# Kernel optimization log

Measured on AMD Instinct MI355X. Metric: run time of the kernel, lower is better.

Reference implementation:

```python
import jax, jax.numpy as jnp
import numpy as np

H = 19  # input_size == hidden_size

def setup_inputs() -> dict:
    key = jax.random.key(0)
    ks = jax.random.split(key, 7)
    seq_len, batch = 2048, 1024
    s = 1.0 / np.sqrt(H)  # PyTorch default uniform(-1/sqrt(H), 1/sqrt(H))
    x = jax.random.normal(ks[0], (seq_len, batch, H), dtype=jnp.float32)
    W_ih = jax.random.uniform(ks[1], (3 * H, H), jnp.float32, -s, s)
    W_hh = jax.random.uniform(ks[2], (3 * H, H), jnp.float32, -s, s)
    b_ih = jax.random.uniform(ks[3], (3 * H,), jnp.float32, -s, s)
    b_hh = jax.random.uniform(ks[4], (3 * H,), jnp.float32, -s, s)
    W_out = jax.random.uniform(ks[5], (1, H), jnp.float32, -s, s)
    b_out = jax.random.uniform(ks[6], (1,), jnp.float32, -s, s)
    return {"x": x, "W_ih": W_ih, "W_hh": W_hh, "b_ih": b_ih,
            "b_hh": b_hh, "W_out": W_out, "b_out": b_out}

def _gru(x, W_ih, W_hh, b_ih, b_hh):
    # Precompute all input projections in one big GEMM: [T, B, 3H]
    xg = jnp.einsum('tbi,gi->tbg', x, W_ih) + b_ih
    Whr, Whz, Whn = W_hh[:H], W_hh[H:2*H], W_hh[2*H:]
    bhr, bhz, bhn = b_hh[:H], b_hh[H:2*H], b_hh[2*H:]
    h0 = jnp.zeros(x.shape[1:2] + (H,), dtype=x.dtype)

    def step(h, xg_t):
        xr, xz, xn = xg_t[:, :H], xg_t[:, H:2*H], xg_t[:, 2*H:]
        r = jax.nn.sigmoid(xr + h @ Whr.T + bhr)
        z = jax.nn.sigmoid(xz + h @ Whz.T + bhz)
        n = jnp.tanh(xn + r * (h @ Whn.T + bhn))
        h_new = (1.0 - z) * n + z * h
        return h_new, h_new

    _, r_out = jax.lax.scan(step, h0, xg)  # r_out: [T, B, H]
    return r_out

def reference(x, W_ih, W_hh, b_ih, b_hh, W_out, b_out):
    r_out = _gru(x, W_ih, W_hh, b_ih, b_hh)
    return r_out @ W_out.T + b_out  # [T, B, 1]
```

## Files before the change

kernel.cpp:

```cpp
#include <hip/hip_runtime.h>
#include <math.h>

#define HH 19
#define NG 57
#define SL 64
#define NB 1024
#define TT 2048

typedef float v2f __attribute__((ext_vector_type(2)));
typedef float v4f __attribute__((ext_vector_type(4)));
typedef unsigned u2 __attribute__((ext_vector_type(2)));

__device__ __forceinline__ float rlf(float v, int l) {
  return __uint_as_float(__builtin_amdgcn_readlane(__float_as_uint(v), l));
}
__device__ __forceinline__ float frcp(float v) { return __builtin_amdgcn_rcpf(v); }
__device__ __forceinline__ float fexp2(float v) {
#if __has_builtin(__builtin_amdgcn_exp2f)
  return __builtin_amdgcn_exp2f(v);
#else
  return exp2f(v);
#endif
}
__device__ __forceinline__ unsigned short f2h(float f) {
  return __builtin_bit_cast(unsigned short, (_Float16)f);
}
__device__ __forceinline__ float h2f(unsigned short u) {
  return (float)__builtin_bit_cast(_Float16, u);
}
__device__ __forceinline__ v2f mk2(float a, float b) { v2f r; r.x = a; r.y = b; return r; }
__device__ __forceinline__ v2f vfma(v2f a, v2f b, v2f c) {
#if __has_builtin(__builtin_elementwise_fma)
  return __builtin_elementwise_fma(a, b, c);
#else
  v2f r; r.x = fmaf(a.x, b.x, c.x); r.y = fmaf(a.y, b.y, c.y); return r;
#endif
}

#if __has_builtin(__builtin_amdgcn_permlane32_swap)
#define HAVE_PLS 1
__device__ __forceinline__ u2 pls(float x) {
  unsigned u = __float_as_uint(x);
  return __builtin_amdgcn_permlane32_swap(u, u, false, false);
}
#else
#define HAVE_PLS 0
#endif

__global__ __launch_bounds__(256) void xg_proj3(
    const float* __restrict__ x, const float* __restrict__ Wih,
    const float* __restrict__ bih, const float* __restrict__ bhh,
    unsigned short* __restrict__ xg)
{
  const int lane = threadIdx.x & 63;
  const int wv = __builtin_amdgcn_readfirstlane((int)(threadIdx.x >> 6));
  const int g = lane < NG ? lane : NG - 1;
  const float L2E = 1.4426950408889634f;
  const float scale = (g < 2 * HH) ? -L2E : 2.0f * L2E;

  float w[HH];
#pragma unroll
  for (int k = 0; k < HH; ++k) w[k] = Wih[g * HH + k] * scale;
  const float cbv = (bih[g] + (g < 2 * HH ? bhh[g] : 0.0f)) * scale;

  const size_t pair0 = ((size_t)blockIdx.x * 4 + wv) * 64;
  for (int p = 0; p < 64; ++p) {
    const size_t pair = pair0 + p;
    const float* __restrict__ xr = x + pair * HH;
    float a = cbv;
#pragma unroll
    for (int k = 0; k < HH; ++k) a = fmaf(xr[k], w[k], a);
    xg[pair * SL + lane] = f2h(a);
  }
}

__global__ void __launch_bounds__(64)
__attribute__((amdgpu_waves_per_eu(1, 1)))
gru_rec3(const unsigned short* __restrict__ xg, const float* __restrict__ Whh,
         const float* __restrict__ bhh, const float* __restrict__ Wout,
         const float* __restrict__ bout, float* __restrict__ out)
{
  __shared__ __align__(16) float hsh[64];
  const int b = blockIdx.x;
  const int lane = threadIdx.x;
  const float L2E = 1.4426950408889634f;

  int row;
  if (lane < 32)      row = lane;
  else if (lane < 51) row = lane + 6;
  else if (lane < 57) row = lane - 19;
  else                row = 37;
  const bool isn = (row >= 2 * HH);
  const float s = isn ? (2.0f * L2E) : -L2E;

  v2f wh2[10], wo2[10];
#pragma unroll
  for (int j = 0; j < 10; ++j) {
    const int k0 = 2 * j, k1 = 2 * j + 1;
    wh2[j].x = s * Whh[row * HH + k0];
    wh2[j].y = (k1 < HH) ? s * Whh[row * HH + k1] : 0.0f;
    wo2[j].x = Wout[k0];
    wo2[j].y = (k1 < HH) ? Wout[k1] : 0.0f;
  }
  const float dinit = isn ? (2.0f * L2E * bhh[row]) : 0.0f;
  const float bo = bout[0];

  const int il = lane < HH ? lane : HH - 1;
  const int zaddr = ((il < 13) ? (19 + il) : (38 + il)) * 4;

#if HAVE_PLS
  bool loIsX;
  {
    unsigned l = (unsigned)lane;
    u2 pr = __builtin_amdgcn_permlane32_swap(l, l, false, false);
    loIsX = ((unsigned)__builtin_amdgcn_readlane((int)pr.x, 32) < 32u);
  }
#define LOBCAST(val, dst) do { u2 _s = pls(val);                        \
    dst = __uint_as_float(loIsX ? _s.x : _s.y); } while (0)
#define HIBCAST(val, dst) do { u2 _s = pls(val);                        \
    dst = __uint_as_float(loIsX ? _s.y : _s.x); } while (0)
#else
  const int loaddr = (lane & 31) * 4;
  const int hiaddr = ((lane & 31) | 32) * 4;
#define LOBCAST(val, dst) dst = __uint_as_float((unsigned)              \
    __builtin_amdgcn_ds_bpermute(loaddr, (int)__float_as_uint(val)))
#define HIBCAST(val, dst) dst = __uint_as_float((unsigned)              \
    __builtin_amdgcn_ds_bpermute(hiaddr, (int)__float_as_uint(val)))
#endif

  float h = 0.0f;
  v2f shA[10], shB[10];
#pragma unroll
  for (int j = 0; j < 10; ++j) { shA[j] = mk2(0.f, 0.f); shB[j] = mk2(0.f, 0.f); }

  const unsigned short* __restrict__ xb = xg + (size_t)b * SL + row;
#define LOADX(dst, trow) do { dst = xb[(size_t)(trow) * (NB * SL)]; } while (0)

  unsigned short s0, s1, s2, s3, s4, s5, s6, s7;
  LOADX(s0, 0); LOADX(s1, 1); LOADX(s2, 2); LOADX(s3, 3);
  LOADX(s4, 4); LOADX(s5, 5); LOADX(s6, 6); LOADX(s7, 7);

#define OPROJ(sh, ovar) do {                                            \
    v2f _oA = mk2(bo, 0.f), _oB = mk2(0.f, 0.f);                        \
    _Pragma("unroll")                                                   \
    for (int _j = 0; _j < 5; ++_j)  _oA = vfma(sh[_j], wo2[_j], _oA);   \
    _Pragma("unroll")                                                   \
    for (int _j = 5; _j < 10; ++_j) _oB = vfma(sh[_j], wo2[_j], _oB);   \
    const v2f _ov = _oA + _oB;                                          \
    ovar = _ov.x + _ov.y;                                               \
  } while (0)

#define BODY(tcur, slot, shC, shP, ovar) do {                           \
     \
    hsh[lane] = (lane < HH) ? h : 0.0f;                                 \
    const v4f q0 = *(const v4f*)&hsh[0];                                \
    const v4f q1 = *(const v4f*)&hsh[4];                                \
    const v4f q2 = *(const v4f*)&hsh[8];                                \
    const v4f q3 = *(const v4f*)&hsh[12];                               \
    const v4f q4 = *(const v4f*)&hsh[16];                               \
    const float xv = h2f(slot);                                         \
    { const int _tl = ((tcur) + 8 < TT) ? (tcur) + 8 : TT - 1;          \
      LOADX(slot, _tl); }                                               \
                     \
    OPROJ(shP, ovar);                                                   \
    shC[0] = mk2(q0.x, q0.y); shC[1] = mk2(q0.z, q0.w);                 \
    shC[2] = mk2(q1.x, q1.y); shC[3] = mk2(q1.z, q1.w);                 \
    shC[4] = mk2(q2.x, q2.y); shC[5] = mk2(q2.z, q2.w);                 \
    shC[6] = mk2(q3.x, q3.y); shC[7] = mk2(q3.z, q3.w);                 \
    shC[8] = mk2(q4.x, q4.y); shC[9] = mk2(q4.z, q4.w);                 \
                                \
    v2f _a0 = mk2(dinit, 0.f), _a1 = mk2(0.f, 0.f);                     \
    _Pragma("unroll")                                                   \
    for (int _j = 0; _j < 5; ++_j)  _a0 = vfma(shC[_j], wh2[_j], _a0);  \
    _Pragma("unroll")                                                   \
    for (int _j = 5; _j < 10; ++_j) _a1 = vfma(shC[_j], wh2[_j], _a1);  \
    const v2f _av = _a0 + _a1;                                          \
    const float preh = _av.x + _av.y;                                   \
    const float pre  = xv + preh;                        \
    const float sig  = frcp(fexp2(pre) + 1.0f);                         \
    const int zzi = __builtin_amdgcn_ds_bpermute(                       \
        zaddr, (int)__float_as_uint(sig));                              \
    float rr; LOBCAST(sig, rr);                                         \
    const float arg = fmaf(rr, preh, xv);                  \
    const float nn = fmaf(-2.0f, frcp(fexp2(arg) + 1.0f), 1.0f);        \
    float nh; HIBCAST(nn, nh);                                          \
    const float zz = __uint_as_float((unsigned)zzi);                    \
    h = fmaf(zz, h - nh, nh);                                           \
  } while (0)

  float o0, o1, o2, o3, o4, o5, o6, o7;
  float* __restrict__ ob = out + b;

  for (int t = 0; t < TT; t += 8) {
    BODY(t + 0, s0, shA, shB, o0);
    BODY(t + 1, s1, shB, shA, o1);
    BODY(t + 2, s2, shA, shB, o2);
    BODY(t + 3, s3, shB, shA, o3);
    BODY(t + 4, s4, shA, shB, o4);
    BODY(t + 5, s5, shB, shA, o5);
    BODY(t + 6, s6, shA, shB, o6);
    BODY(t + 7, s7, shB, shA, o7);
    if (lane == 0) {
      ob[(size_t)(t >= 2 ? t - 2 : 0) * NB] = o0;
      ob[(size_t)(t >= 1 ? t - 1 : 0) * NB] = o1;
      ob[(size_t)(t + 0) * NB] = o2;
      ob[(size_t)(t + 1) * NB] = o3;
      ob[(size_t)(t + 2) * NB] = o4;
      ob[(size_t)(t + 3) * NB] = o5;
      ob[(size_t)(t + 4) * NB] = o6;
      ob[(size_t)(t + 5) * NB] = o7;
    }
  }

  float oe;
  OPROJ(shB, oe);
  if (lane == 0) ob[(size_t)(TT - 2) * NB] = oe;
  hsh[lane] = (lane < HH) ? h : 0.0f;
  {
    const v4f q0 = *(const v4f*)&hsh[0];
    const v4f q1 = *(const v4f*)&hsh[4];
    const v4f q2 = *(const v4f*)&hsh[8];
    const v4f q3 = *(const v4f*)&hsh[12];
    const v4f q4 = *(const v4f*)&hsh[16];
    shA[0] = mk2(q0.x, q0.y); shA[1] = mk2(q0.z, q0.w);
    shA[2] = mk2(q1.x, q1.y); shA[3] = mk2(q1.z, q1.w);
    shA[4] = mk2(q2.x, q2.y); shA[5] = mk2(q2.z, q2.w);
    shA[6] = mk2(q3.x, q3.y); shA[7] = mk2(q3.z, q3.w);
    shA[8] = mk2(q4.x, q4.y); shA[9] = mk2(q4.z, q4.w);
    OPROJ(shA, oe);
    if (lane == 0) ob[(size_t)(TT - 1) * NB] = oe;
  }
#undef LOADX
#undef BODY
#undef OPROJ
#undef LOBCAST
#undef HIBCAST
}

__global__ void __launch_bounds__(64)
__attribute__((amdgpu_waves_per_eu(1, 1)))
gru57_v4(const float* __restrict__ x, const float* __restrict__ Wih,
         const float* __restrict__ Whh, const float* __restrict__ bih,
         const float* __restrict__ bhh, const float* __restrict__ Wout,
         const float* __restrict__ bout, float* __restrict__ out)
{
  const int b = blockIdx.x;
  const int lane = threadIdx.x;
  const float L2E = 1.4426950408889634f;

  int row;
  if (lane < 32)      row = lane;
  else if (lane < 51) row = lane + 6;
  else if (lane < 57) row = lane - 19;
  else                row = 37;
  const bool isn = (row >= 2 * HH);
  const float scale = isn ? (2.0f * L2E) : L2E;

  v2f wx2[10], wh2[10], wo2[10];
#pragma unroll
  for (int j = 0; j < 10; ++j) {
    const int k0 = 2 * j, k1 = 2 * j + 1;
    wx2[j].x = Wih[row * HH + k0] * scale;
    wx2[j].y = (k1 < HH) ? Wih[row * HH + k1] * scale : 0.0f;
    wh2[j].x = Whh[row * HH + k0] * scale;
    wh2[j].y = (k1 < HH) ? Whh[row * HH + k1] * scale : 0.0f;
    wo2[j].x = Wout[k0];
    wo2[j].y = (k1 < HH) ? Wout[k1] : 0.0f;
  }
  const float bxv = bih[row] * scale, bhv = bhh[row] * scale;
  const float ax0 = isn ? bxv : (bxv + bhv);
  const float ah0 = isn ? bhv : 0.0f;
  const float bo  = bout[0];

  const int il = lane < HH ? lane : HH - 1;
  const int zaddr = ((il < 13) ? (19 + il) : (38 + il)) * 4;

#if HAVE_PLS
  bool loIsX;
  {
    unsigned l = (unsigned)lane;
    u2 pr = __builtin_amdgcn_permlane32_swap(l, l, false, false);
    loIsX = ((unsigned)__builtin_amdgcn_readlane((int)pr.x, 32) < 32u);
  }
#define LOBCAST(val, dst) do { u2 _s = pls(val);                        \
    dst = __uint_as_float(loIsX ? _s.x : _s.y); } while (0)
#define HIBCAST(val, dst) do { u2 _s = pls(val);                        \
    dst = __uint_as_float(loIsX ? _s.y : _s.x); } while (0)
#else
  const int loaddr = (lane & 31) * 4;
  const int hiaddr = ((lane & 31) | 32) * 4;
#define LOBCAST(val, dst) dst = __uint_as_float((unsigned)              \
    __builtin_amdgcn_ds_bpermute(loaddr, (int)__float_as_uint(val)))
#define HIBCAST(val, dst) dst = __uint_as_float((unsigned)              \
    __builtin_amdgcn_ds_bpermute(hiaddr, (int)__float_as_uint(val)))
#endif

  float h = 0.0f;
  v2f sh2[10];
#pragma unroll
  for (int j = 0; j < 10; ++j) sh2[j] = mk2(0.f, 0.f);

  const int kx = lane < HH ? lane : HH - 1;
  const float* __restrict__ xbase = x + (size_t)b * HH + kx;

#define LOADXF(dst, trow) do { dst = xbase[(size_t)(trow) * (NB * HH)]; } while (0)
#define XBCAST(slot, xu) do {                                           \
    _Pragma("unroll")                                                   \
    for (int _j = 0; _j < 9; ++_j) {                                    \
      xu[_j].x = rlf(slot, 2 * _j);                                     \
      xu[_j].y = rlf(slot, 2 * _j + 1);                                 \
    }                                                                   \
    xu[9].x = rlf(slot, 18); xu[9].y = 0.0f;                            \
  } while (0)
#define XDOT(xu, dstvar) do {                                           \
    v2f _aA = mk2(ax0, 0.0f), _aB = mk2(0.0f, 0.0f);                    \
    _Pragma("unroll")                                                   \
    for (int _j = 0; _j < 5; ++_j)  _aA = vfma(xu[_j], wx2[_j], _aA);   \
    _Pragma("unroll")                                                   \
    for (int _j = 5; _j < 10; ++_j) _aB = vfma(xu[_j], wx2[_j], _aB);   \
    const v2f _s = _aA + _aB;                                           \
    dstvar = _s.x + _s.y;                                               \
  } while (0)

  float xlA, xlB, xlC, xlD;
  LOADXF(xlA, 0); LOADXF(xlB, 1); LOADXF(xlC, 2); LOADXF(xlD, 3);
  float prex;
  { v2f xu0[10]; XBCAST(xlA, xu0); XDOT(xu0, prex); }

#define BODYF(tcur, nslot, lslot) do {                                  \
    v2f ahA = mk2(ah0, 0.0f), ahB = mk2(0.0f, 0.0f);                    \
    _Pragma("unroll")                                                   \
    for (int _j = 0; _j < 5; ++_j)  ahA = vfma(sh2[_j], wh2[_j], ahA);  \
    _Pragma("unroll")                                                   \
    for (int _j = 5; _j < 10; ++_j) ahB = vfma(sh2[_j], wh2[_j], ahB);  \
    float prexN;                                                        \
    { v2f _xu[10]; XBCAST(nslot, _xu); XDOT(_xu, prexN); }              \
    { const int _tl = ((tcur) + 4 < TT) ? (tcur) + 4 : TT - 1;          \
      LOADXF(lslot, _tl); }                                             \
    const v2f ahv = ahA + ahB;                                          \
    const float preh = ahv.x + ahv.y;                                   \
    const float pre  = prex + preh;                                     \
    const float sig  = frcp(1.0f + fexp2(-pre));                        \
    const int zzi = __builtin_amdgcn_ds_bpermute(                       \
        zaddr, (int)__float_as_uint(sig));                              \
    float rr; LOBCAST(sig, rr);                                         \
    const float npre = fmaf(rr, preh, prex);                            \
    const float nn = fmaf(-2.0f, frcp(fexp2(npre) + 1.0f), 1.0f);       \
    float nh; HIBCAST(nn, nh);                                          \
    const float zz = __uint_as_float((unsigned)zzi);                    \
    h = fmaf(zz, h - nh, nh);                                           \
    _Pragma("unroll")                                                   \
    for (int _j = 0; _j < 9; ++_j) {                                    \
      sh2[_j].x = rlf(h, 2 * _j);                                       \
      sh2[_j].y = rlf(h, 2 * _j + 1);                                   \
    }                                                                   \
    sh2[9].x = rlf(h, 18); sh2[9].y = 0.0f;                             \
    v2f oA = mk2(bo, 0.0f), oB = mk2(0.0f, 0.0f);                       \
    _Pragma("unroll")                                                   \
    for (int _j = 0; _j < 5; ++_j)  oA = vfma(sh2[_j], wo2[_j], oA);    \
    _Pragma("unroll")                                                   \
    for (int _j = 5; _j < 10; ++_j) oB = vfma(sh2[_j], wo2[_j], oB);    \
    const v2f ov = oA + oB;                                             \
    if (lane == 0) out[(size_t)(tcur) * NB + b] = ov.x + ov.y;          \
    prex = prexN;                                                       \
  } while (0)

  for (int t = 0; t < TT; t += 4) {
    BODYF(t + 0, xlB, xlA);
    BODYF(t + 1, xlC, xlB);
    BODYF(t + 2, xlD, xlC);
    BODYF(t + 3, xlA, xlD);
  }

#undef LOADXF
#undef XBCAST
#undef XDOT
#undef BODYF
#undef LOBCAST
#undef HIBCAST
}

extern "C" void kernel_launch(void* const* d_in, const int* in_sizes, int n_in,
                              void* d_out, int out_size, void* d_ws, size_t ws_size,
                              hipStream_t stream) {
  const float* x    = (const float*)d_in[0];
  const float* Wih  = (const float*)d_in[1];
  const float* Whh  = (const float*)d_in[2];
  const float* bih  = (const float*)d_in[3];
  const float* bhh  = (const float*)d_in[4];
  const float* Wout = (const float*)d_in[5];
  const float* bout = (const float*)d_in[6];
  float* out = (float*)d_out;

  const size_t need = (size_t)TT * NB * SL * sizeof(unsigned short);
  if (ws_size >= need) {
    unsigned short* xgws = (unsigned short*)d_ws;
    xg_proj3<<<dim3((TT * NB) / 256), dim3(256), 0, stream>>>(
        x, Wih, bih, bhh, xgws);
    gru_rec3<<<dim3(NB), dim3(64), 0, stream>>>(
        xgws, Whh, bhh, Wout, bout, out);
  } else {
    gru57_v4<<<dim3(NB), dim3(64), 0, stream>>>(
        x, Wih, Whh, bih, bhh, Wout, bout, out);
  }
}
```

Measured before the change: 627.2 us.

## Restructure GRU recurrence lanes, broadcast h via readlane, stage projection through LDS

The projection kernel now stages x through shared memory, computes all 57 gates per thread (one pair per thread), and writes the result out coalesced through an LDS transpose, instead of reading x row-wise per lane. The recurrence kernel changes its lane mapping: each lane computes both an r/n row and a z row, so z no longer needs a cross-lane bpermute. h is broadcast to all lanes with readlane instead of an LDS store and reload. The output projection runs on the current h, which shifts the store indices by one. The cost is about twice the FMAs per lane and 19 scalar readlanes per step on the serial critical path.

```diff
diff --git a/kernel.cpp b/kernel.cpp
--- a/kernel.cpp
+++ b/kernel.cpp
@@ -8,7 +8,6 @@
 #define TT 2048
 
 typedef float v2f __attribute__((ext_vector_type(2)));
-typedef float v4f __attribute__((ext_vector_type(4)));
 typedef unsigned u2 __attribute__((ext_vector_type(2)));
 
 __device__ __forceinline__ float rlf(float v, int l) {
@@ -47,66 +46,81 @@
 #define HAVE_PLS 0
 #endif
 
-__global__ __launch_bounds__(256) void xg_proj3(
+__global__ __launch_bounds__(256) void xg_proj4(
     const float* __restrict__ x, const float* __restrict__ Wih,
     const float* __restrict__ bih, const float* __restrict__ bhh,
     unsigned short* __restrict__ xg)
 {
-  const int lane = threadIdx.x & 63;
-  const int wv = __builtin_amdgcn_readfirstlane((int)(threadIdx.x >> 6));
-  const int g = lane < NG ? lane : NG - 1;
+  __shared__ __align__(16) float ls[256 * 33];
+  const int tid = threadIdx.x;
+  const size_t pair0 = (size_t)blockIdx.x * 256;
   const float L2E = 1.4426950408889634f;
-  const float scale = (g < 2 * HH) ? -L2E : 2.0f * L2E;
-
-  float w[HH];
-#pragma unroll
-  for (int k = 0; k < HH; ++k) w[k] = Wih[g * HH + k] * scale;
-  const float cbv = (bih[g] + (g < 2 * HH ? bhh[g] : 0.0f)) * scale;
-
-  const size_t pair0 = ((size_t)blockIdx.x * 4 + wv) * 64;
-  for (int p = 0; p < 64; ++p) {
-    const size_t pair = pair0 + p;
-    const float* __restrict__ xr = x + pair * HH;
-    float a = cbv;
-#pragma unroll
-    for (int k = 0; k < HH; ++k) a = fmaf(xr[k], w[k], a);
-    xg[pair * SL + lane] = f2h(a);
+
+  {
+    const float* __restrict__ src = x + pair0 * HH;
+#pragma unroll
+    for (int j = 0; j < HH; ++j) ls[j * 256 + tid] = src[j * 256 + tid];
+  }
+  __syncthreads();
+
+  float xv[HH];
+#pragma unroll
+  for (int k = 0; k < HH; ++k) xv[k] = ls[tid * HH + k];
+  __syncthreads();
+
+  unsigned short* __restrict__ lsh = (unsigned short*)ls;
+#pragma unroll 1
+  for (int g = 0; g < NG; ++g) {
+    float a = bih[g] + ((g < 2 * HH) ? bhh[g] : 0.0f);
+#pragma unroll
+    for (int k = 0; k < HH; ++k) a = fmaf(xv[k], Wih[g * HH + k], a);
+    a *= (g < 2 * HH) ? -L2E : (2.0f * L2E);
+    lsh[tid * 66 + g] = f2h(a);
+  }
+#pragma unroll
+  for (int g = NG; g < SL; ++g) lsh[tid * 66 + g] = 0;
+  __syncthreads();
+
+  const unsigned* __restrict__ lsd = (const unsigned*)ls;
+  unsigned* __restrict__ xgd = (unsigned*)xg;
+#pragma unroll
+  for (int i = 0; i < 32; ++i) {
+    const int D = tid + i * 256;
+    xgd[pair0 * 32 + D] = lsd[(D >> 5) * 33 + (D & 31)];
   }
 }
 
 __global__ void __launch_bounds__(64)
 __attribute__((amdgpu_waves_per_eu(1, 1)))
-gru_rec3(const unsigned short* __restrict__ xg, const float* __restrict__ Whh,
+gru_rec5(const unsigned short* __restrict__ xg, const float* __restrict__ Whh,
          const float* __restrict__ bhh, const float* __restrict__ Wout,
          const float* __restrict__ bout, float* __restrict__ out)
 {
-  __shared__ __align__(16) float hsh[64];
   const int b = blockIdx.x;
   const int lane = threadIdx.x;
   const float L2E = 1.4426950408889634f;
 
-  int row;
-  if (lane < 32)      row = lane;
-  else if (lane < 51) row = lane + 6;
-  else if (lane < 57) row = lane - 19;
-  else                row = 37;
-  const bool isn = (row >= 2 * HH);
-  const float s = isn ? (2.0f * L2E) : -L2E;
-
-  v2f wh2[10], wo2[10];
+  const bool isN = (lane >= 32 && lane < 32 + HH);
+  int rowA;
+  if (lane < HH)  rowA = lane;
+  else if (isN)   rowA = 2 * HH + (lane - 32);
+  else            rowA = 0;
+  const int rowB = (lane < HH) ? (HH + lane) : HH;
+
+  const float sA = isN ? (2.0f * L2E) : -L2E;
+  v2f wA2[10], wB2[10], wo2[10];
 #pragma unroll
   for (int j = 0; j < 10; ++j) {
     const int k0 = 2 * j, k1 = 2 * j + 1;
-    wh2[j].x = s * Whh[row * HH + k0];
-    wh2[j].y = (k1 < HH) ? s * Whh[row * HH + k1] : 0.0f;
+    wA2[j].x = sA * Whh[rowA * HH + k0];
+    wA2[j].y = (k1 < HH) ? sA * Whh[rowA * HH + k1] : 0.0f;
+    wB2[j].x = -L2E * Whh[rowB * HH + k0];
+    wB2[j].y = (k1 < HH) ? -L2E * Whh[rowB * HH + k1] : 0.0f;
     wo2[j].x = Wout[k0];
     wo2[j].y = (k1 < HH) ? Wout[k1] : 0.0f;
   }
-  const float dinit = isn ? (2.0f * L2E * bhh[row]) : 0.0f;
+  const float dinitA = isN ? (2.0f * L2E * bhh[rowA]) : 0.0f;
   const float bo = bout[0];
-
-  const int il = lane < HH ? lane : HH - 1;
-  const int zaddr = ((il < 13) ? (19 + il) : (38 + il)) * 4;
 
 #if HAVE_PLS
   bool loIsX;
@@ -129,16 +143,20 @@
 #endif
 
   float h = 0.0f;
-  v2f shA[10], shB[10];
-#pragma unroll
-  for (int j = 0; j < 10; ++j) { shA[j] = mk2(0.f, 0.f); shB[j] = mk2(0.f, 0.f); }
-
-  const unsigned short* __restrict__ xb = xg + (size_t)b * SL + row;
-#define LOADX(dst, trow) do { dst = xb[(size_t)(trow) * (NB * SL)]; } while (0)
-
-  unsigned short s0, s1, s2, s3, s4, s5, s6, s7;
-  LOADX(s0, 0); LOADX(s1, 1); LOADX(s2, 2); LOADX(s3, 3);
-  LOADX(s4, 4); LOADX(s5, 5); LOADX(s6, 6); LOADX(s7, 7);
+  v2f sh2[10];
+#pragma unroll
+  for (int j = 0; j < 10; ++j) sh2[j] = mk2(0.f, 0.f);
+
+  const unsigned short* __restrict__ xaA = xg + (size_t)b * SL + rowA;
+  const unsigned short* __restrict__ xaB = xg + (size_t)b * SL + rowB;
+#define LOADA(dst, t) dst = xaA[(size_t)(t) * (NB * SL)]
+#define LOADB(dst, t) dst = xaB[(size_t)(t) * (NB * SL)]
+
+  unsigned short a0,a1,a2,a3,a4,a5,a6,a7, b0,b1,b2,b3,b4,b5,b6,b7;
+  LOADA(a0,0); LOADB(b0,0); LOADA(a1,1); LOADB(b1,1);
+  LOADA(a2,2); LOADB(b2,2); LOADA(a3,3); LOADB(b3,3);
+  LOADA(a4,4); LOADB(b4,4); LOADA(a5,5); LOADB(b5,5);
+  LOADA(a6,6); LOADB(b6,6); LOADA(a7,7); LOADB(b7,7);
 
 #define OPROJ(sh, ovar) do {                                            \
     v2f _oA = mk2(bo, 0.f), _oB = mk2(0.f, 0.f);                        \
@@ -150,87 +168,65 @@
     ovar = _ov.x + _ov.y;                                               \
   } while (0)
 
-#define BODY(tcur, slot, shC, shP, ovar) do {                           \
-     \
-    hsh[lane] = (lane < HH) ? h : 0.0f;                                 \
-    const v4f q0 = *(const v4f*)&hsh[0];                                \
-    const v4f q1 = *(const v4f*)&hsh[4];                                \
-    const v4f q2 = *(const v4f*)&hsh[8];                                \
-    const v4f q3 = *(const v4f*)&hsh[12];                               \
-    const v4f q4 = *(const v4f*)&hsh[16];                               \
-    const float xv = h2f(slot);                                         \
+#define BODY(tcur, as_, bs_, ovar) do {                                 \
+    const float xvA = h2f(as_);                                         \
+    const float xvB = h2f(bs_);                                         \
     { const int _tl = ((tcur) + 8 < TT) ? (tcur) + 8 : TT - 1;          \
-      LOADX(slot, _tl); }                                               \
-                     \
-    OPROJ(shP, ovar);                                                   \
-    shC[0] = mk2(q0.x, q0.y); shC[1] = mk2(q0.z, q0.w);                 \
-    shC[2] = mk2(q1.x, q1.y); shC[3] = mk2(q1.z, q1.w);                 \
-    shC[4] = mk2(q2.x, q2.y); shC[5] = mk2(q2.z, q2.w);                 \
-    shC[6] = mk2(q3.x, q3.y); shC[7] = mk2(q3.z, q3.w);                 \
-    shC[8] = mk2(q4.x, q4.y); shC[9] = mk2(q4.z, q4.w);                 \
-                                \
-    v2f _a0 = mk2(dinit, 0.f), _a1 = mk2(0.f, 0.f);                     \
-    _Pragma("unroll")                                                   \
-    for (int _j = 0; _j < 5; ++_j)  _a0 = vfma(shC[_j], wh2[_j], _a0);  \
-    _Pragma("unroll")                                                   \
-    for (int _j = 5; _j < 10; ++_j) _a1 = vfma(shC[_j], wh2[_j], _a1);  \
-    const v2f _av = _a0 + _a1;                                          \
-    const float preh = _av.x + _av.y;                                   \
-    const float pre  = xv + preh;                        \
-    const float sig  = frcp(fexp2(pre) + 1.0f);                         \
-    const int zzi = __builtin_amdgcn_ds_bpermute(                       \
-        zaddr, (int)__float_as_uint(sig));                              \
-    float rr; LOBCAST(sig, rr);                                         \
-    const float arg = fmaf(rr, preh, xv);                  \
+      LOADA(as_, _tl); LOADB(bs_, _tl); }                               \
+    v2f aA0 = mk2(dinitA, 0.f), aA1 = mk2(0.f, 0.f);                    \
+    v2f aB0 = mk2(xvB, 0.f),    aB1 = mk2(0.f, 0.f);                    \
+    _Pragma("unroll")                                                   \
+    for (int _j = 0; _j < 5; ++_j) {                                    \
+      aA0 = vfma(sh2[_j], wA2[_j], aA0);                                \
+      aB0 = vfma(sh2[_j], wB2[_j], aB0);                                \
+    }                                                                   \
+    _Pragma("unroll")                                                   \
+    for (int _j = 5; _j < 10; ++_j) {                                   \
+      aA1 = vfma(sh2[_j], wA2[_j], aA1);                                \
+      aB1 = vfma(sh2[_j], wB2[_j], aB1);                                \
+    }                                                                   \
+    const v2f avA = aA0 + aA1, avB = aB0 + aB1;                         \
+    const float preA = avA.x + avA.y;          \
+    const float preB = avB.x + avB.y;         \
+    const float sig1 = frcp(fexp2(xvA + preA) + 1.0f);         \
+    float rr; LOBCAST(sig1, rr);                    \
+    const float zz = frcp(fexp2(preB) + 1.0f);                 \
+    OPROJ(sh2, ovar);                             \
+    const float arg = fmaf(rr, preA, xvA);                              \
     const float nn = fmaf(-2.0f, frcp(fexp2(arg) + 1.0f), 1.0f);        \
-    float nh; HIBCAST(nn, nh);                                          \
-    const float zz = __uint_as_float((unsigned)zzi);                    \
+    float nh; HIBCAST(nn, nh);                      \
     h = fmaf(zz, h - nh, nh);                                           \
+    _Pragma("unroll")                                                   \
+    for (int _j = 0; _j < 9; ++_j)                                      \
+      sh2[_j] = mk2(rlf(h, 2 * _j), rlf(h, 2 * _j + 1));                \
+    sh2[9] = mk2(rlf(h, 18), 0.0f);                                     \
   } while (0)
 
   float o0, o1, o2, o3, o4, o5, o6, o7;
   float* __restrict__ ob = out + b;
 
   for (int t = 0; t < TT; t += 8) {
-    BODY(t + 0, s0, shA, shB, o0);
-    BODY(t + 1, s1, shB, shA, o1);
-    BODY(t + 2, s2, shA, shB, o2);
-    BODY(t + 3, s3, shB, shA, o3);
-    BODY(t + 4, s4, shA, shB, o4);
-    BODY(t + 5, s5, shB, shA, o5);
-    BODY(t + 6, s6, shA, shB, o6);
-    BODY(t + 7, s7, shB, shA, o7);
+    BODY(t + 0, a0, b0, o0); BODY(t + 1, a1, b1, o1);
+    BODY(t + 2, a2, b2, o2); BODY(t + 3, a3, b3, o3);
+    BODY(t + 4, a4, b4, o4); BODY(t + 5, a5, b5, o5);
+    BODY(t + 6, a6, b6, o6); BODY(t + 7, a7, b7, o7);
     if (lane == 0) {
-      ob[(size_t)(t >= 2 ? t - 2 : 0) * NB] = o0;
-      ob[(size_t)(t >= 1 ? t - 1 : 0) * NB] = o1;
-      ob[(size_t)(t + 0) * NB] = o2;
-      ob[(size_t)(t + 1) * NB] = o3;
-      ob[(size_t)(t + 2) * NB] = o4;
-      ob[(size_t)(t + 3) * NB] = o5;
-      ob[(size_t)(t + 4) * NB] = o6;
-      ob[(size_t)(t + 5) * NB] = o7;
+      ob[(size_t)((t > 0) ? t - 1 : 0) * NB] = o0;
+      ob[(size_t)(t + 0) * NB] = o1;
+      ob[(size_t)(t + 1) * NB] = o2;
+      ob[(size_t)(t + 2) * NB] = o3;
+      ob[(size_t)(t + 3) * NB] = o4;
+      ob[(size_t)(t + 4) * NB] = o5;
+      ob[(size_t)(t + 5) * NB] = o6;
+      ob[(size_t)(t + 6) * NB] = o7;
     }
   }
-
   float oe;
-  OPROJ(shB, oe);
-  if (lane == 0) ob[(size_t)(TT - 2) * NB] = oe;
-  hsh[lane] = (lane < HH) ? h : 0.0f;
-  {
-    const v4f q0 = *(const v4f*)&hsh[0];
-    const v4f q1 = *(const v4f*)&hsh[4];
-    const v4f q2 = *(const v4f*)&hsh[8];
-    const v4f q3 = *(const v4f*)&hsh[12];
-    const v4f q4 = *(const v4f*)&hsh[16];
-    shA[0] = mk2(q0.x, q0.y); shA[1] = mk2(q0.z, q0.w);
-    shA[2] = mk2(q1.x, q1.y); shA[3] = mk2(q1.z, q1.w);
-    shA[4] = mk2(q2.x, q2.y); shA[5] = mk2(q2.z, q2.w);
-    shA[6] = mk2(q3.x, q3.y); shA[7] = mk2(q3.z, q3.w);
-    shA[8] = mk2(q4.x, q4.y); shA[9] = mk2(q4.z, q4.w);
-    OPROJ(shA, oe);
-    if (lane == 0) ob[(size_t)(TT - 1) * NB] = oe;
-  }
-#undef LOADX
+  OPROJ(sh2, oe);
+  if (lane == 0) ob[(size_t)(TT - 1) * NB] = oe;
+
+#undef LOADA
+#undef LOADB
 #undef BODY
 #undef OPROJ
 #undef LOBCAST
@@ -395,9 +391,9 @@
   const size_t need = (size_t)TT * NB * SL * sizeof(unsigned short);
   if (ws_size >= need) {
     unsigned short* xgws = (unsigned short*)d_ws;
-    xg_proj3<<<dim3((TT * NB) / 256), dim3(256), 0, stream>>>(
+    xg_proj4<<<dim3((TT * NB) / 256), dim3(256), 0, stream>>>(
         x, Wih, bih, bhh, xgws);
-    gru_rec3<<<dim3(NB), dim3(64), 0, stream>>>(
+    gru_rec5<<<dim3(NB), dim3(64), 0, stream>>>(
         xgws, Whh, bhh, Wout, bout, out);
   } else {
     gru57_v4<<<dim3(NB), dim3(64), 0, stream>>>(
```

Measured after the change: 724.6 us. 1.16x slower.
